# Performance work log

Measured on AMD Instinct MI355X. Metric: run time of the kernel, lower is better.

## Reference

```python
import jax, jax.numpy as jnp
import numpy as np

B, L, D, H = 32, 384, 512, 16
DK = D // H  # head dim = 32


def setup_inputs() -> dict:
    key = jax.random.key(0)
    ks = jax.random.split(key, 8)
    w = lambda k, shape: jax.random.normal(k, shape, dtype=jnp.float32) * 0.02
    return {
        "Q":   jax.random.normal(ks[0], (B, L, D), dtype=jnp.float32),
        "Wq":  w(ks[1], (D, D)),  "bq": jnp.zeros((D,), jnp.float32),
        "Wk":  w(ks[2], (D, D)),  "bk": jnp.zeros((D,), jnp.float32),
        "Wv":  w(ks[3], (D, D)),  "bv": jnp.zeros((D,), jnp.float32),
        "Wql": w(ks[4], (DK, DK)), "bql": jnp.zeros((DK,), jnp.float32),
        "Wkl": w(ks[5], (DK, DK)), "bkl": jnp.zeros((DK,), jnp.float32),
        "Wo":  w(ks[6], (D, D)),  "bo": jnp.zeros((D,), jnp.float32),
        # segment_len is None -> upper triangular ones (diagonal=0), a fixed buffer
        "triu": jnp.triu(jnp.ones((L, L), jnp.float32)),
    }


def reference(Q, Wq, bq, Wk, bk, Wv, bv, Wql, bql, Wkl, bkl, Wo, bo, triu):
    scale = DK ** -0.5
    # QKV projections -> [B, H, L, DK]
    q = (Q @ Wq + bq).reshape(B, L, H, DK).transpose(0, 2, 1, 3)
    k = (Q @ Wk + bk).reshape(B, L, H, DK).transpose(0, 2, 1, 3)
    v = (Q @ Wv + bv).reshape(B, L, H, DK).transpose(0, 2, 1, 3)
    # weighted mask (left variant): extra per-head L/K projections over head dim
    qL = q @ Wql + bql
    kL = k @ Wkl + bkl
    phi = jax.nn.softmax(jnp.einsum('bhqd,bhkd->bhqk', qL, kL) * scale, axis=-1)
    m_s = phi @ triu  # [B, H, L, L]
    # standard attention, softmax, then elementwise multiply with m_s
    scores = jnp.einsum('bhqd,bhkd->bhqk', q, k) * scale
    attn = jax.nn.softmax(scores, axis=-1) * m_s
    out = jnp.einsum('bhqk,bhkd->bhqd', attn, v)
    out = out.transpose(0, 2, 1, 3).reshape(B, L, D)
    return out @ Wo + bo  # [B, L, D]
```

## Files before the change

### kernel.cpp

```cpp
#include <hip/hip_runtime.h>
#include <hip/hip_bf16.h>

#define Bsz 32
#define Lsz 384
#define Dsz 512
#define Hn  16
#define DKs 32
#define SCALEF 0.17677669529663687f
#define QSC (0.17677669529663687f * 1.4426950408889634f)

typedef __attribute__((ext_vector_type(8)))  short bf16x8;
typedef __attribute__((ext_vector_type(4)))  float f32x4;
typedef __attribute__((ext_vector_type(16))) float f32x16;

__device__ __forceinline__ unsigned pk2(float a, float b) {
    union { __hip_bfloat16 h; unsigned short u; } ca, cb;
    ca.h = __float2bfloat16(a);
    cb.h = __float2bfloat16(b);
    return (unsigned)ca.u | ((unsigned)cb.u << 16);
}
__device__ __forceinline__ unsigned short bfbits(float a) {
    union { __hip_bfloat16 h; unsigned short u; } c;
    c.h = __float2bfloat16(a);
    return c.u;
}
__device__ __forceinline__ void gload_lds16(const void* g, void* l) {
    __builtin_amdgcn_global_load_lds((const __attribute__((address_space(1))) void*)g,
                                     (__attribute__((address_space(3))) void*)l, 16, 0, 0);
}
__device__ __forceinline__ float fexp2(float x) { return __builtin_amdgcn_exp2f(x); }
__device__ __forceinline__ void plswap(unsigned& a, unsigned& b) {
    asm("v_permlane32_swap_b32 %0, %1" : "+v"(a), "+v"(b));
}
__device__ __forceinline__ float xhalf(float t, int h5) {
    unsigned a = __float_as_uint(t);
    unsigned b;
    asm("v_mov_b32 %0, %1\n\t"
        "v_permlane32_swap_b32 %1, %0"
        : "=&v"(b), "+v"(a));
    return h5 ? __uint_as_float(a) : __uint_as_float(b);
}

__global__ __launch_bounds__(256) void convq_kernel(
    const float* __restrict__ src, unsigned short* __restrict__ dst)
{
    size_t i = ((size_t)blockIdx.x * 256 + threadIdx.x) * 8;
    float4 a = *(const float4*)(src + i);
    float4 b = *(const float4*)(src + i + 4);
    *(uint4*)(dst + i) = make_uint4(pk2(a.x, a.y), pk2(a.z, a.w),
                                    pk2(b.x, b.y), pk2(b.z, b.w));
}

__global__ __launch_bounds__(256) void wprep_t(
    const float* __restrict__ W0, const float* __restrict__ W1,
    const float* __restrict__ W2, const float* __restrict__ W3,
    unsigned short* __restrict__ dst)
{
    const int z = blockIdx.z;
    const float* W = (z == 0) ? W0 : (z == 1) ? W1 : (z == 2) ? W2 : W3;
    unsigned short* out = dst + (size_t)z * 512 * 512;
    __shared__ float Ls[64][65];
    const int tid = threadIdx.x;
    const int k0 = blockIdx.x * 64, n0 = blockIdx.y * 64;
    #pragma unroll
    for (int i = 0; i < 4; ++i) {
        int c = i * 256 + tid;
        int r = c >> 4, c4 = c & 15;
        float4 v = *(const float4*)&W[(size_t)(k0 + r) * 512 + n0 + c4 * 4];
        Ls[r][c4 * 4 + 0] = v.x; Ls[r][c4 * 4 + 1] = v.y;
        Ls[r][c4 * 4 + 2] = v.z; Ls[r][c4 * 4 + 3] = v.w;
    }
    __syncthreads();
    #pragma unroll
    for (int i = 0; i < 2; ++i) {
        int c = i * 256 + tid;
        int n = c >> 3, kc = c & 7;
        unsigned u[4];
        #pragma unroll
        for (int p = 0; p < 4; ++p)
            u[p] = pk2(Ls[kc * 8 + 2 * p][n], Ls[kc * 8 + 2 * p + 1][n]);
        *(uint4*)&out[(size_t)(n0 + n) * 512 + k0 + kc * 8] =
            make_uint4(u[0], u[1], u[2], u[3]);
    }
}

template <int MODE, int NT>
__global__ __launch_bounds__(256) void mm_kernel(
    const unsigned short* __restrict__ A, const unsigned short* __restrict__ WT,
    const float* __restrict__ bias, const float* __restrict__ bias2,
    const float* __restrict__ bias3, void* __restrict__ outv)
{
    __shared__ __align__(16) unsigned short Asm[2][128 * 64];
    __shared__ __align__(16) unsigned short Bsm[2][64 * 64];

    const int tid = threadIdx.x, lane = tid & 63, w = tid >> 6;
    const int r16 = lane & 15, qd = lane >> 4;
    const int wm = w >> 1, wn = w & 1;

    const int bid = blockIdx.x;
    const int xcd = bid & 7, loc = bid >> 3;
    const int mt = xcd * 12 + loc / NT;
    const int nt = loc % NT;
    const int m0 = mt * 128, n0 = nt * 64;

    f32x4 acc[4][2];
    #pragma unroll
    for (int mi = 0; mi < 4; ++mi)
        #pragma unroll
        for (int ni = 0; ni < 2; ++ni) acc[mi][ni] = (f32x4){0.f, 0.f, 0.f, 0.f};

    const int rA = (tid >> 3) & 127;
    auto stage = [&](int k0, int bi) {
        #pragma unroll
        for (int i = 0; i < 4; ++i) {
            int c = i * 256 + tid;
            int r = c >> 3, sl = c & 7;
            int gc = (sl ^ (r & 7)) * 8;
            gload_lds16(A + ((size_t)(m0 + r) * 512 + k0 + gc),
                        &Asm[bi][(i * 256 + w * 64) * 8]);
            if (i < 2)
                gload_lds16(WT + ((size_t)(n0 + r) * 512 + k0 + gc),
                            &Bsm[bi][(i * 256 + w * 64) * 8]);
        }
    };
    (void)rA;

    stage(0, 0);
    __syncthreads();
    int cur = 0;
    for (int kt = 0; kt < 8; ++kt) {
        if (kt < 7) stage((kt + 1) * 64, cur ^ 1);

        bf16x8 af[4][2], bfr[2][2];
        #pragma unroll
        for (int mi = 0; mi < 4; ++mi) {
            int row = wm * 64 + mi * 16 + r16;
            #pragma unroll
            for (int ks = 0; ks < 2; ++ks) {
                int sl = (ks * 4 + qd) ^ (row & 7);
                af[mi][ks] = *(const bf16x8*)&Asm[cur][row * 64 + sl * 8];
            }
        }
        #pragma unroll
        for (int ni = 0; ni < 2; ++ni) {
            int row = wn * 32 + ni * 16 + r16;
            #pragma unroll
            for (int ks = 0; ks < 2; ++ks) {
                int sl = (ks * 4 + qd) ^ (row & 7);
                bfr[ni][ks] = *(const bf16x8*)&Bsm[cur][row * 64 + sl * 8];
            }
        }
        #pragma unroll
        for (int ks = 0; ks < 2; ++ks)
            #pragma unroll
            for (int mi = 0; mi < 4; ++mi)
                #pragma unroll
                for (int ni = 0; ni < 2; ++ni)
                    acc[mi][ni] = __builtin_amdgcn_mfma_f32_16x16x32_bf16(
                        af[mi][ks], bfr[ni][ks], acc[mi][ni], 0, 0, 0);

        __syncthreads();
        cur ^= 1;
    }

    const int b = m0 / Lsz;
    const int l0 = m0 - b * Lsz;
    const size_t PLANE = (size_t)Bsz * Hn * Lsz * DKs;

    if (MODE == 0) {
        #pragma unroll
        for (int ni = 0; ni < 2; ++ni) {
            int n = n0 + wn * 32 + ni * 16 + r16;
            int t = n >> 9;
            int n9 = n & 511;
            int hh = n9 >> 5, dk = n9 & 31;
            if (t == 2) {
                unsigned short* o = (unsigned short*)outv + 4 * PLANE;
                float bv_ = bias3[n9];
                size_t base = ((size_t)(b * Hn + hh) * DKs + dk) * Lsz;
                #pragma unroll
                for (int mi = 0; mi < 4; ++mi) {
                    int l = l0 + wm * 64 + mi * 16 + qd * 4;
                    ushort4 st;
                    st.x = bfbits(acc[mi][ni][0] + bv_);
                    st.y = bfbits(acc[mi][ni][1] + bv_);
                    st.z = bfbits(acc[mi][ni][2] + bv_);
                    st.w = bfbits(acc[mi][ni][3] + bv_);
                    *(ushort4*)&o[base + l] = st;
                }
            } else {
                float sc = t ? 1.f : QSC;
                float bv_ = t ? bias2[n9] : bias[n9];
                unsigned short* o = (unsigned short*)outv + (size_t)t * PLANE;
                size_t base = ((size_t)(b * Hn + hh) * Lsz) * DKs + dk;
                #pragma unroll
                for (int mi = 0; mi < 4; ++mi)
                    #pragma unroll
                    for (int rr = 0; rr < 4; ++rr) {
                        int l = l0 + wm * 64 + mi * 16 + qd * 4 + rr;
                        o[base + (size_t)l * DKs] = bfbits((acc[mi][ni][rr] + bv_) * sc);
                    }
            }
        }
    } else {
        float* o = (float*)outv;
        #pragma unroll
        for (int ni = 0; ni < 2; ++ni) {
            int n = n0 + wn * 32 + ni * 16 + r16;
            float bv_ = bias[n];
            #pragma unroll
            for (int mi = 0; mi < 4; ++mi)
                #pragma unroll
                for (int rr = 0; rr < 4; ++rr) {
                    int m = m0 + wm * 64 + mi * 16 + qd * 4 + rr;
                    o[(size_t)m * 512 + n] = acc[mi][ni][rr] + bv_;
                }
        }
    }
}

__global__ __launch_bounds__(256) void lproj_mfma(
    const unsigned short* __restrict__ qsrc, const unsigned short* __restrict__ ksrc,
    const float* __restrict__ Wql, const float* __restrict__ bql,
    const float* __restrict__ Wkl, const float* __restrict__ bkl,
    unsigned short* __restrict__ qLdst, unsigned short* __restrict__ kLdst)
{
    const int t = blockIdx.y;
    const unsigned short* src = t ? ksrc : qsrc;
    const float* W = t ? Wkl : Wql;
    const float* bias = t ? bkl : bql;
    const float bscale = t ? 1.f : QSC;
    unsigned short* dst = t ? kLdst : qLdst;

    const int lane = threadIdx.x & 63, w = threadIdx.x >> 6;
    const int d = lane & 31, h5 = lane >> 5;

    union { unsigned u[4]; bf16x8 v; } B1, B2;
    #pragma unroll
    for (int i = 0; i < 4; ++i) {
        B1.u[i] = pk2(W[(8 * h5 + 2 * i) * 32 + d],      W[(8 * h5 + 2 * i + 1) * 32 + d]);
        B2.u[i] = pk2(W[(16 + 8 * h5 + 2 * i) * 32 + d], W[(16 + 8 * h5 + 2 * i + 1) * 32 + d]);
    }
    const float bv = bias[d] * bscale;
    f32x16 binit;
    #pragma unroll
    for (int r = 0; r < 16; ++r) binit[r] = bv;

    const int base_row = blockIdx.x * 256 + w * 64;
    #pragma unroll
    for (int g = 0; g < 2; ++g) {
        const int rowbase = base_row + g * 32;
        const unsigned short* sp = src + (size_t)(rowbase + d) * 32;
        bf16x8 A1 = *(const bf16x8*)(sp + 8 * h5);
        bf16x8 A2 = *(const bf16x8*)(sp + 16 + 8 * h5);
        f32x16 acc = binit;
        acc = __builtin_amdgcn_mfma_f32_32x32x16_bf16(A1, B1.v, acc, 0, 0, 0);
        acc = __builtin_amdgcn_mfma_f32_32x32x16_bf16(A2, B2.v, acc, 0, 0, 0);
        #pragma unroll
        for (int r = 0; r < 16; ++r) {
            int i = (r & 3) + 8 * (r >> 2) + 4 * h5;
            dst[(size_t)(rowbase + i) * 32 + d] = bfbits(acc[r]);
        }
    }
}

__global__ __launch_bounds__(128) void attn_mfma(
    const unsigned short* __restrict__ qs, const unsigned short* __restrict__ kp,
    const unsigned short* __restrict__ qLp, const unsigned short* __restrict__ kLp,
    const unsigned short* __restrict__ vT, unsigned short* __restrict__ ao)
{
    const int lane = threadIdx.x & 63, w = threadIdx.x >> 6;
    const int q31 = lane & 31, h5 = lane >> 5;

    const int bid = blockIdx.x;
    const int flat = (bid & 7) * 384 + (bid >> 3);
    const int qt2 = flat % 6;
    const int rest = flat / 6;
    const int h = rest & 15;
    const int b = rest >> 4;
    const size_t bh = (size_t)(b * Hn + h);
    const int q0 = (qt2 * 2 + w) * 32;

    const unsigned short* qb  = qs  + bh * (Lsz * DKs);
    const unsigned short* kb  = kp  + bh * (Lsz * DKs);
    const unsigned short* qLb = qLp + bh * (Lsz * DKs);
    const unsigned short* kLb = kLp + bh * (Lsz * DKs);
    const unsigned short* vb  = vT  + bh * (DKs * Lsz);

    const int qrow = q0 + q31;
    const unsigned short* qrp  = qb  + qrow * DKs;
    const unsigned short* qLrp = qLb + qrow * DKs;
    bf16x8 qB1  = *(const bf16x8*)(qrp + 8 * h5);
    bf16x8 qB2  = *(const bf16x8*)(qrp + 16 + 8 * h5);
    bf16x8 qLB1 = *(const bf16x8*)(qLrp + 8 * h5);
    bf16x8 qLB2 = *(const bf16x8*)(qLrp + 16 + 8 * h5);

    f32x16 o = {};
    const f32x16 Z = {};
    float s2sum = 0.f, carry = 0.f;

    for (int k0 = 0; k0 < Lsz; k0 += 32) {
        const unsigned short* kr  = kb  + (k0 + q31) * DKs;
        const unsigned short* kLr = kLb + (k0 + q31) * DKs;
        bf16x8 kA1  = *(const bf16x8*)(kr + 8 * h5);
        bf16x8 kA2  = *(const bf16x8*)(kr + 16 + 8 * h5);
        bf16x8 kLA1 = *(const bf16x8*)(kLr + 8 * h5);
        bf16x8 kLA2 = *(const bf16x8*)(kLr + 16 + 8 * h5);
        const unsigned short* vr = vb + q31 * Lsz + k0;
        bf16x8 vA1 = *(const bf16x8*)(vr + 8 * h5);
        bf16x8 vA2 = *(const bf16x8*)(vr + 16 + 8 * h5);

        f32x16 S1 = __builtin_amdgcn_mfma_f32_32x32x16_bf16(kLA1, qLB1, Z, 0, 0, 0);
        S1 = __builtin_amdgcn_mfma_f32_32x32x16_bf16(kLA2, qLB2, S1, 0, 0, 0);
        f32x16 S2 = __builtin_amdgcn_mfma_f32_32x32x16_bf16(kA1, qB1, Z, 0, 0, 0);
        S2 = __builtin_amdgcn_mfma_f32_32x32x16_bf16(kA2, qB2, S2, 0, 0, 0);

        float e1[16], e2[16];
        #pragma unroll
        for (int r = 0; r < 16; ++r) {
            e1[r] = fexp2(S1[r]);
            e2[r] = fexp2(S2[r]);
        }

        float p[16];
        #pragma unroll
        for (int j = 0; j < 4; ++j) {
            p[4*j+0] = e1[4*j+0];
            p[4*j+1] = p[4*j+0] + e1[4*j+1];
            p[4*j+2] = p[4*j+1] + e1[4*j+2];
            p[4*j+3] = p[4*j+2] + e1[4*j+3];
        }
        float X[4], U[4];
        #pragma unroll
        for (int j = 0; j < 4; ++j) {
            X[j] = xhalf(p[4*j+3], h5);
            U[j] = p[4*j+3] + X[j];
        }
        float Sp1 = U[0], Sp2 = U[0] + U[1], Sp3 = Sp2 + U[2];
        float Spre[4] = {0.f, Sp1, Sp2, Sp3};
        float P[16];
        #pragma unroll
        for (int j = 0; j < 4; ++j) {
            float base = carry + Spre[j] + (h5 ? X[j] : 0.f);
            #pragma unroll
            for (int i = 0; i < 4; ++i)
                P[4*j+i] = e2[4*j+i] * (base + p[4*j+i]);
        }
        carry += Sp3 + U[3];

        float t0 = (e2[0] + e2[1]) + (e2[2] + e2[3]);
        float t1 = (e2[4] + e2[5]) + (e2[6] + e2[7]);
        float t2 = (e2[8] + e2[9]) + (e2[10] + e2[11]);
        float t3 = (e2[12] + e2[13]) + (e2[14] + e2[15]);
        s2sum += (t0 + t1) + (t2 + t3);

        unsigned pk[8];
        #pragma unroll
        for (int j = 0; j < 4; ++j) {
            pk[2*j]   = pk2(P[4*j],   P[4*j+1]);
            pk[2*j+1] = pk2(P[4*j+2], P[4*j+3]);
        }
        unsigned a0 = pk[0], b0 = pk[2]; plswap(a0, b0);
        unsigned a1 = pk[1], b1 = pk[3]; plswap(a1, b1);
        unsigned a2 = pk[4], b2 = pk[6]; plswap(a2, b2);
        unsigned a3 = pk[5], b3 = pk[7]; plswap(a3, b3);
        union { unsigned u[4]; bf16x8 v; } B1, B2;
        B1.u[0] = a0; B1.u[1] = a1; B1.u[2] = b0; B1.u[3] = b1;
        B2.u[0] = a2; B2.u[1] = a3; B2.u[2] = b2; B2.u[3] = b3;

        o = __builtin_amdgcn_mfma_f32_32x32x16_bf16(vA1, B1.v, o, 0, 0, 0);
        o = __builtin_amdgcn_mfma_f32_32x32x16_bf16(vA2, B2.v, o, 0, 0, 0);
    }

    float s2 = s2sum + xhalf(s2sum, h5);
    float nm = __builtin_amdgcn_rcpf(carry * s2);
    unsigned short* op = ao + ((size_t)(b * Lsz) + q0 + q31) * Dsz + h * DKs + 4 * h5;
    #pragma unroll
    for (int j = 0; j < 4; ++j) {
        *(uint2*)(op + 8 * j) = make_uint2(pk2(o[4*j] * nm,   o[4*j+1] * nm),
                                           pk2(o[4*j+2] * nm, o[4*j+3] * nm));
    }
}

extern "C" void kernel_launch(void* const* d_in, const int* in_sizes, int n_in,
                              void* d_out, int out_size, void* d_ws, size_t ws_size,
                              hipStream_t stream) {
    const float* Q   = (const float*)d_in[0];
    const float* Wq  = (const float*)d_in[1];
    const float* bq  = (const float*)d_in[2];
    const float* Wk  = (const float*)d_in[3];
    const float* bk  = (const float*)d_in[4];
    const float* Wv  = (const float*)d_in[5];
    const float* bv  = (const float*)d_in[6];
    const float* Wql = (const float*)d_in[7];
    const float* bql = (const float*)d_in[8];
    const float* Wkl = (const float*)d_in[9];
    const float* bkl = (const float*)d_in[10];
    const float* Wo  = (const float*)d_in[11];
    const float* bo  = (const float*)d_in[12];

    const size_t PLANE = (size_t)Bsz * Hn * Lsz * DKs;
    unsigned short* P0     = (unsigned short*)d_ws;
    unsigned short* vT_p   = P0 + 4 * PLANE;
    unsigned short* ao     = vT_p + PLANE;
    unsigned short* Qbf    = ao + PLANE;
    unsigned short* WT_all = Qbf + PLANE;

    convq_kernel<<<3072, 256, 0, stream>>>(Q, Qbf);
    wprep_t<<<dim3(8, 8, 4), 256, 0, stream>>>(Wq, Wk, Wv, Wo, WT_all);
    mm_kernel<0, 24><<<2304, 256, 0, stream>>>(Qbf, WT_all, bq, bk, bv, P0);
    lproj_mfma<<<dim3(768, 2), 256, 0, stream>>>(P0, P0 + PLANE, Wql, bql, Wkl, bkl,
                                                 P0 + 2 * PLANE, P0 + 3 * PLANE);
    attn_mfma<<<3072, 128, 0, stream>>>(P0, P0 + PLANE, P0 + 2 * PLANE,
                                        P0 + 3 * PLANE, vT_p, ao);
    mm_kernel<3, 8><<<768, 256, 0, stream>>>(ao, WT_all + (size_t)1536 * 512, bo, bo, bo, d_out);
}
```

Baseline: 114.5 us.

## Fold Wql·Wklᵀ into a single q-side projection, drop kL plane

Precomputes M = Wql·Wklᵀ plus the bias cross-terms in a tiny kernel, so qL·kLᵀ becomes (q·M + bql·Wklᵀ)·kᵀ plus a per-query constant. The k-side projection pass and the kL plane disappear. The attention loop reuses the already-loaded k fragments for both score MFMAs, which halves the key-side global loads for the mask scores. This adds a one-block prep kernel and a per-row constant computed from q, and it changes bf16 rounding, since the product is rounded once instead of qL and kL each being rounded.

```diff
diff --git a/kernel.cpp b/kernel.cpp
--- a/kernel.cpp
+++ b/kernel.cpp
@@ -40,6 +40,9 @@
         : "=&v"(b), "+v"(a));
     return h5 ? __uint_as_float(a) : __uint_as_float(b);
 }
+__device__ __forceinline__ float bf2f(short s) {
+    return __uint_as_float(((unsigned)(unsigned short)s) << 16);
+}
 
 __global__ __launch_bounds__(256) void convq_kernel(
     const float* __restrict__ src, unsigned short* __restrict__ dst)
@@ -84,6 +87,38 @@
     }
 }
 
+__global__ __launch_bounds__(256) void wprep_l(
+    const float* __restrict__ Wql, const float* __restrict__ bql,
+    const float* __restrict__ Wkl, const float* __restrict__ bkl,
+    float* __restrict__ out)
+{
+    const int t = threadIdx.x;
+    #pragma unroll
+    for (int i = 0; i < 4; ++i) {
+        int idx = t * 4 + i;
+        int e = idx >> 5, d = idx & 31;
+        float s = 0.f;
+        #pragma unroll
+        for (int j = 0; j < 32; ++j) s += Wql[e * 32 + j] * Wkl[d * 32 + j];
+        out[idx] = s;
+    }
+    if (t < 32) {
+        float s = 0.f;
+        #pragma unroll
+        for (int j = 0; j < 32; ++j) s += bql[j] * Wkl[t * 32 + j];
+        out[1024 + t] = s;
+        float v = 0.f;
+        #pragma unroll
+        for (int d = 0; d < 32; ++d) v += Wql[t * 32 + d] * bkl[d];
+        out[1056 + t] = v;
+    }
+    if (t == 0) {
+        float s = 0.f;
+        for (int d = 0; d < 32; ++d) s += bql[d] * bkl[d];
+        out[1088] = s * QSC;
+    }
+}
+
 template <int MODE, int NT>
 __global__ __launch_bounds__(256) void mm_kernel(
     const unsigned short* __restrict__ A, const unsigned short* __restrict__ WT,
@@ -109,7 +144,6 @@
         #pragma unroll
         for (int ni = 0; ni < 2; ++ni) acc[mi][ni] = (f32x4){0.f, 0.f, 0.f, 0.f};
 
-    const int rA = (tid >> 3) & 127;
     auto stage = [&](int k0, int bi) {
         #pragma unroll
         for (int i = 0; i < 4; ++i) {
@@ -123,7 +157,6 @@
                             &Bsm[bi][(i * 256 + w * 64) * 8]);
         }
     };
-    (void)rA;
 
     stage(0, 0);
     __syncthreads();
@@ -220,18 +253,9 @@
 }
 
 __global__ __launch_bounds__(256) void lproj_mfma(
-    const unsigned short* __restrict__ qsrc, const unsigned short* __restrict__ ksrc,
-    const float* __restrict__ Wql, const float* __restrict__ bql,
-    const float* __restrict__ Wkl, const float* __restrict__ bkl,
-    unsigned short* __restrict__ qLdst, unsigned short* __restrict__ kLdst)
-{
-    const int t = blockIdx.y;
-    const unsigned short* src = t ? ksrc : qsrc;
-    const float* W = t ? Wkl : Wql;
-    const float* bias = t ? bkl : bql;
-    const float bscale = t ? 1.f : QSC;
-    unsigned short* dst = t ? kLdst : qLdst;
-
+    const unsigned short* __restrict__ src, const float* __restrict__ W,
+    const float* __restrict__ bias, unsigned short* __restrict__ dst)
+{
     const int lane = threadIdx.x & 63, w = threadIdx.x >> 6;
     const int d = lane & 31, h5 = lane >> 5;
 
@@ -241,7 +265,7 @@
         B1.u[i] = pk2(W[(8 * h5 + 2 * i) * 32 + d],      W[(8 * h5 + 2 * i + 1) * 32 + d]);
         B2.u[i] = pk2(W[(16 + 8 * h5 + 2 * i) * 32 + d], W[(16 + 8 * h5 + 2 * i + 1) * 32 + d]);
     }
-    const float bv = bias[d] * bscale;
+    const float bv = bias[d] * QSC;
     f32x16 binit;
     #pragma unroll
     for (int r = 0; r < 16; ++r) binit[r] = bv;
@@ -266,7 +290,7 @@
 
 __global__ __launch_bounds__(128) void attn_mfma(
     const unsigned short* __restrict__ qs, const unsigned short* __restrict__ kp,
-    const unsigned short* __restrict__ qLp, const unsigned short* __restrict__ kLp,
+    const unsigned short* __restrict__ qAp, const float* __restrict__ lconst,
     const unsigned short* __restrict__ vT, unsigned short* __restrict__ ao)
 {
     const int lane = threadIdx.x & 63, w = threadIdx.x >> 6;
@@ -283,35 +307,43 @@
 
     const unsigned short* qb  = qs  + bh * (Lsz * DKs);
     const unsigned short* kb  = kp  + bh * (Lsz * DKs);
-    const unsigned short* qLb = qLp + bh * (Lsz * DKs);
-    const unsigned short* kLb = kLp + bh * (Lsz * DKs);
+    const unsigned short* qAb = qAp + bh * (Lsz * DKs);
     const unsigned short* vb  = vT  + bh * (DKs * Lsz);
 
     const int qrow = q0 + q31;
     const unsigned short* qrp  = qb  + qrow * DKs;
-    const unsigned short* qLrp = qLb + qrow * DKs;
+    const unsigned short* qArp = qAb + qrow * DKs;
     bf16x8 qB1  = *(const bf16x8*)(qrp + 8 * h5);
     bf16x8 qB2  = *(const bf16x8*)(qrp + 16 + 8 * h5);
-    bf16x8 qLB1 = *(const bf16x8*)(qLrp + 8 * h5);
-    bf16x8 qLB2 = *(const bf16x8*)(qLrp + 16 + 8 * h5);
+    bf16x8 qAB1 = *(const bf16x8*)(qArp + 8 * h5);
+    bf16x8 qAB2 = *(const bf16x8*)(qArp + 16 + 8 * h5);
+
+    const float* vcp = lconst + 1056;
+    float partial = 0.f;
+    #pragma unroll
+    for (int i = 0; i < 8; ++i) {
+        partial += bf2f(qB1[i]) * vcp[8 * h5 + i];
+        partial += bf2f(qB2[i]) * vcp[16 + 8 * h5 + i];
+    }
+    const float c_q = partial + xhalf(partial, h5) + lconst[1088];
+    f32x16 Cc;
+    #pragma unroll
+    for (int r = 0; r < 16; ++r) Cc[r] = c_q;
 
     f32x16 o = {};
     const f32x16 Z = {};
     float s2sum = 0.f, carry = 0.f;
 
     for (int k0 = 0; k0 < Lsz; k0 += 32) {
-        const unsigned short* kr  = kb  + (k0 + q31) * DKs;
-        const unsigned short* kLr = kLb + (k0 + q31) * DKs;
-        bf16x8 kA1  = *(const bf16x8*)(kr + 8 * h5);
-        bf16x8 kA2  = *(const bf16x8*)(kr + 16 + 8 * h5);
-        bf16x8 kLA1 = *(const bf16x8*)(kLr + 8 * h5);
-        bf16x8 kLA2 = *(const bf16x8*)(kLr + 16 + 8 * h5);
+        const unsigned short* kr = kb + (k0 + q31) * DKs;
+        bf16x8 kA1 = *(const bf16x8*)(kr + 8 * h5);
+        bf16x8 kA2 = *(const bf16x8*)(kr + 16 + 8 * h5);
         const unsigned short* vr = vb + q31 * Lsz + k0;
         bf16x8 vA1 = *(const bf16x8*)(vr + 8 * h5);
         bf16x8 vA2 = *(const bf16x8*)(vr + 16 + 8 * h5);
 
-        f32x16 S1 = __builtin_amdgcn_mfma_f32_32x32x16_bf16(kLA1, qLB1, Z, 0, 0, 0);
-        S1 = __builtin_amdgcn_mfma_f32_32x32x16_bf16(kLA2, qLB2, S1, 0, 0, 0);
+        f32x16 S1 = __builtin_amdgcn_mfma_f32_32x32x16_bf16(kA1, qAB1, Cc, 0, 0, 0);
+        S1 = __builtin_amdgcn_mfma_f32_32x32x16_bf16(kA2, qAB2, S1, 0, 0, 0);
         f32x16 S2 = __builtin_amdgcn_mfma_f32_32x32x16_bf16(kA1, qB1, Z, 0, 0, 0);
         S2 = __builtin_amdgcn_mfma_f32_32x32x16_bf16(kA2, qB2, S2, 0, 0, 0);
 
@@ -405,13 +437,14 @@
     unsigned short* ao     = vT_p + PLANE;
     unsigned short* Qbf    = ao + PLANE;
     unsigned short* WT_all = Qbf + PLANE;
+    float*          lconst = (float*)(WT_all + (size_t)2048 * 512);
 
     convq_kernel<<<3072, 256, 0, stream>>>(Q, Qbf);
     wprep_t<<<dim3(8, 8, 4), 256, 0, stream>>>(Wq, Wk, Wv, Wo, WT_all);
+    wprep_l<<<1, 256, 0, stream>>>(Wql, bql, Wkl, bkl, lconst);
     mm_kernel<0, 24><<<2304, 256, 0, stream>>>(Qbf, WT_all, bq, bk, bv, P0);
-    lproj_mfma<<<dim3(768, 2), 256, 0, stream>>>(P0, P0 + PLANE, Wql, bql, Wkl, bkl,
-                                                 P0 + 2 * PLANE, P0 + 3 * PLANE);
+    lproj_mfma<<<768, 256, 0, stream>>>(P0, lconst, lconst + 1024, P0 + 2 * PLANE);
     attn_mfma<<<3072, 128, 0, stream>>>(P0, P0 + PLANE, P0 + 2 * PLANE,
-                                        P0 + 3 * PLANE, vT_p, ao);
+                                        lconst, vT_p, ao);
     mm_kernel<3, 8><<<768, 256, 0, stream>>>(ao, WT_all + (size_t)1536 * 512, bo, bo, bo, d_out);
 }
```

Measured after the change: 118.5 us. +3.5%, slower.
